# Optimization experiments

Measured on AMD Instinct MI355X. Metric: run time of the kernel, lower is better.

The kernel has to match this reference:

```python
import jax, jax.numpy as jnp
import numpy as np

D_MODEL = 128
N_HEADS = 8
D_HEAD = D_MODEL // N_HEADS
D_EDGE = 32
D_GATE = max(D_EDGE * 2, 64)
N_NODES = 50000
N_EDGES = 800000


def setup_inputs() -> dict:
    key = jax.random.key(0)
    ks = jax.random.split(key, 11)
    s = 1.0 / np.sqrt(D_MODEL)
    se = 1.0 / np.sqrt(D_EDGE)
    sg = 1.0 / np.sqrt(D_GATE)
    return {
        "x": jax.random.normal(ks[0], (N_NODES, D_MODEL), jnp.float32),
        "edge_index": jax.random.randint(ks[1], (2, N_EDGES), 0, N_NODES, jnp.int64) if jax.config.jax_enable_x64 else jax.random.randint(ks[1], (2, N_EDGES), 0, N_NODES, jnp.int32),
        "edge_attr": jax.random.normal(ks[2], (N_EDGES, D_EDGE), jnp.float32),
        "W_q": jax.random.normal(ks[3], (D_MODEL, D_MODEL), jnp.float32) * s,
        "W_k": jax.random.normal(ks[4], (D_MODEL, D_MODEL), jnp.float32) * s,
        "W_v": jax.random.normal(ks[5], (D_MODEL, D_MODEL), jnp.float32) * s,
        "W_o": jax.random.normal(ks[6], (D_MODEL, D_MODEL), jnp.float32) * s,
        "W_ek": jax.random.normal(ks[7], (D_EDGE, D_MODEL), jnp.float32) * se,
        "W_ev": jax.random.normal(ks[8], (D_EDGE, D_MODEL), jnp.float32) * se,
        "W_g1": jax.random.normal(ks[9], (D_EDGE, D_GATE), jnp.float32) * se,
        "W_g2": jax.random.normal(ks[10], (D_GATE, N_HEADS), jnp.float32) * sg,
    }


def reference(x, edge_index, edge_attr, W_q, W_k, W_v, W_o, W_ek, W_ev, W_g1, W_g2):
    N = x.shape[0]
    E = edge_attr.shape[0]
    H, D = N_HEADS, D_HEAD
    src, dst = edge_index[0], edge_index[1]

    q = (x @ W_q).reshape(N, H, D)
    k = (x @ W_k).reshape(N, H, D)
    v = (x @ W_v).reshape(N, H, D)

    # per-edge gather + edge-feature enrichment of K, V
    q_e = q[dst]                                        # [E,H,D]
    k_e = k[src] + (edge_attr @ W_ek).reshape(E, H, D)  # [E,H,D]
    v_e = v[src] + (edge_attr @ W_ev).reshape(E, H, D)  # [E,H,D]

    scale = jnp.asarray(np.sqrt(D), x.dtype)
    gate = jax.nn.silu(edge_attr @ W_g1) @ W_g2         # [E,H]
    scores = jnp.sum(q_e * k_e, axis=-1) / scale + gate  # [E,H]

    # 3-pass scatter segment softmax over destination nodes
    m = jax.ops.segment_max(scores, dst, num_segments=N)   # [N,H]
    exp_s = jnp.exp(scores - m[dst])                        # [E,H]
    denom = jax.ops.segment_sum(exp_s, dst, num_segments=N)  # [N,H]
    att = exp_s / (denom[dst] + 1e-9)                       # [E,H]

    out = jax.ops.segment_sum(att[..., None] * v_e, dst, num_segments=N)  # [N,H,D]
    return out.reshape(N, H * D) @ W_o
```

## Files before the change

kernel.cpp:

```cpp
#include <hip/hip_runtime.h>

#define NN 50000
#define NP 50048
#define NE 800000
#define DM 128
#define NH 8
#define DE 32
#define DG 64
#define MAXDEG 64
#define LOG2E 1.44269504088896f
#define SHIFT 16.0f

typedef __attribute__((ext_vector_type(8))) short bf16x8;
typedef __attribute__((ext_vector_type(4))) float f32x4;

__device__ __forceinline__ unsigned short f2bf(float f) {
    unsigned u = __float_as_uint(f);
    unsigned r = u + 0x7FFFu + ((u >> 16) & 1u);
    return (unsigned short)(r >> 16);
}

__device__ __forceinline__ float red16(float x) {
    float v = x;
    int t;
    t = __builtin_amdgcn_update_dpp(0, __float_as_int(v), 0xB1, 0xF, 0xF, true);
    v += __int_as_float(t);
    t = __builtin_amdgcn_update_dpp(0, __float_as_int(v), 0x4E, 0xF, 0xF, true);
    v += __int_as_float(t);
    t = __builtin_amdgcn_update_dpp(0, __float_as_int(v), 0x141, 0xF, 0xF, true);
    v += __int_as_float(t);
    t = __builtin_amdgcn_update_dpp(0, __float_as_int(v), 0x140, 0xF, 0xF, true);
    v += __int_as_float(t);
    return v;
}

__global__ void k_prep(const float* __restrict__ x, unsigned short* __restrict__ xh,
                       const float* __restrict__ Wq, const float* __restrict__ Wk,
                       const float* __restrict__ Wv, unsigned short* __restrict__ wt,
                       const float* __restrict__ Wo, unsigned short* __restrict__ wto,
                       const float* __restrict__ Wek, float* __restrict__ WekT,
                       int* __restrict__ cnt) {
    int idx = blockIdx.x * 256 + threadIdx.x;
    if (idx < NP * DM / 4) {
        float4 t = (idx < NN * DM / 4) ? ((const float4*)x)[idx] : make_float4(0.f, 0.f, 0.f, 0.f);
        ushort4 o;
        o.x = f2bf(t.x); o.y = f2bf(t.y); o.z = f2bf(t.z); o.w = f2bf(t.w);
        ((ushort4*)xh)[idx] = o;
    }
    if (idx < 3 * DM * DM) {
        int m = idx >> 14, rem = idx & 16383, c = rem >> 7, kk = rem & 127;
        const float* W = m == 0 ? Wq : (m == 1 ? Wk : Wv);
        wt[idx] = f2bf(W[kk * DM + c]);
    }
    if (idx < DM * DM) {
        int c = idx >> 7, kk = idx & 127;
        wto[idx] = f2bf(Wo[kk * DM + c]);
    }
    if (idx < DE * DM) {
        int d = idx >> 5, i = idx & 31;
        WekT[idx] = Wek[i * DM + d];
    }
    if (idx < NN) cnt[idx] = 0;
}

__global__ __launch_bounds__(256) void k_qkv(
    const unsigned short* __restrict__ xh, const unsigned short* __restrict__ wt,
    float* __restrict__ q, unsigned* __restrict__ kvp) {
    int lane = threadIdx.x & 63;
    int w = threadIdx.x >> 6;
    int rt = blockIdx.x * 64 + w * 16;
    int cl = lane & 15;
    int kc = (lane >> 4) * 8;
    bf16x8 a[4];
    #pragma unroll
    for (int ks = 0; ks < 4; ++ks)
        a[ks] = *(const bf16x8*)(xh + (size_t)(rt + cl) * DM + ks * 32 + kc);
    int r0w = rt + (lane >> 4) * 4;
    #pragma unroll
    for (int m = 0; m < 3; ++m) {
        const unsigned short* wtm = wt + m * DM * DM;
        f32x4 acc[8];
        #pragma unroll
        for (int j = 0; j < 8; ++j) acc[j] = (f32x4){0.f, 0.f, 0.f, 0.f};
        #pragma unroll
        for (int j = 0; j < 8; ++j) {
            #pragma unroll
            for (int ks = 0; ks < 4; ++ks) {
                bf16x8 b = *(const bf16x8*)(wtm + (size_t)(j * 16 + cl) * DM + ks * 32 + kc);
                acc[j] = __builtin_amdgcn_mfma_f32_16x16x32_bf16(a[ks], b, acc[j], 0, 0, 0);
            }
        }
        if (m == 0) {
            #pragma unroll
            for (int j = 0; j < 8; ++j)
                #pragma unroll
                for (int r = 0; r < 4; ++r)
                    q[(size_t)(r0w + r) * DM + j * 16 + cl] = acc[j][r];
        } else {
            #pragma unroll
            for (int j = 0; j < 4; ++j)
                #pragma unroll
                for (int r = 0; r < 4; ++r) {
                    unsigned pk = (unsigned)f2bf(acc[j][r]) | ((unsigned)f2bf(acc[j + 4][r]) << 16);
                    kvp[(size_t)(r0w + r) * DM + 2 * (j * 16 + cl) + (m - 1)] = pk;
                }
        }
    }
}

__global__ __launch_bounds__(256) void k_qwek(
    const float* __restrict__ q, const float* __restrict__ WekT,
    unsigned* __restrict__ qwekh) {
    int t = threadIdx.x & 127;
    int sub = threadIdx.x >> 7;
    int h = t >> 4, i2 = t & 15;
    float wk0[16], wk1[16];
    #pragma unroll
    for (int d = 0; d < 16; ++d) {
        wk0[d] = WekT[(h * 16 + d) * 32 + 2 * i2];
        wk1[d] = WekT[(h * 16 + d) * 32 + 2 * i2 + 1];
    }
    for (int n = blockIdx.x * 2 + sub; n < NN; n += gridDim.x * 2) {
        const float4* qr = (const float4*)(q + (size_t)n * DM + h * 16);
        float a0 = 0.f, a1 = 0.f;
        #pragma unroll
        for (int c = 0; c < 4; ++c) {
            float4 qq = qr[c];
            a0 += qq.x * wk0[4*c] + qq.y * wk0[4*c+1] + qq.z * wk0[4*c+2] + qq.w * wk0[4*c+3];
            a1 += qq.x * wk1[4*c] + qq.y * wk1[4*c+1] + qq.z * wk1[4*c+2] + qq.w * wk1[4*c+3];
        }
        a0 *= (0.25f * LOG2E);
        a1 *= (0.25f * LOG2E);
        qwekh[(size_t)n * 128 + h * 16 + i2] = (unsigned)f2bf(a0) | ((unsigned)f2bf(a1) << 16);
    }
}

__global__ __launch_bounds__(256) void k_edge(
    const float* __restrict__ ea,
    const float* __restrict__ Wg1, const float* __restrict__ Wg2,
    const int* __restrict__ ei, int* __restrict__ cnt,
    int2* __restrict__ eb, float2* __restrict__ g2) {
    int e = blockIdx.x * 256 + threadIdx.x;
    float eav[DE];
    {
        const float4* p4 = (const float4*)(ea + (size_t)e * DE);
        #pragma unroll
        for (int c = 0; c < DE / 4; ++c) {
            float4 t = p4[c];
            eav[4*c+0] = t.x; eav[4*c+1] = t.y; eav[4*c+2] = t.z; eav[4*c+3] = t.w;
        }
    }
    float out[NH] = {0.f, 0.f, 0.f, 0.f, 0.f, 0.f, 0.f, 0.f};
    #pragma unroll
    for (int half = 0; half < 2; ++half) {
        const int j0 = half * 32;
        float acc[32];
        #pragma unroll
        for (int j = 0; j < 32; ++j) acc[j] = 0.f;
        #pragma unroll 2
        for (int i = 0; i < DE; ++i) {
            const float* __restrict__ wrow = Wg1 + i * DG + j0;
            float a = eav[i];
            #pragma unroll
            for (int j = 0; j < 32; ++j) acc[j] += a * wrow[j];
        }
        #pragma unroll 2
        for (int j = 0; j < 32; ++j) {
            float h = acc[j];
            float s = __fdividef(h, 1.f + __expf(-h));
            const float* __restrict__ w2r = Wg2 + (j0 + j) * NH;
            #pragma unroll
            for (int hh = 0; hh < NH; ++hh) out[hh] += s * w2r[hh];
        }
    }
    #pragma unroll
    for (int hh = 0; hh < 4; ++hh)
        g2[(size_t)e * 4 + hh] = make_float2(out[hh] * LOG2E - SHIFT, out[hh + 4] * LOG2E - SHIFT);
    int src = ei[e], dst = ei[NE + e];
    int slot = atomicAdd(&cnt[dst], 1);
    if (slot < MAXDEG) eb[(size_t)dst * MAXDEG + slot] = make_int2(e, src);
}

#define ECOMP(KV, EAV, G, QA, QB, QWA, QWB, LA, LB, AA, AB, E0, E1, E2, E3) {     \
    unsigned kw = (unsigned)(KV), vw = (unsigned)((KV) >> 32);                    \
    float kA = __uint_as_float(kw << 16);                                         \
    float kB = __uint_as_float(kw & 0xFFFF0000u);                                 \
    float vA = __uint_as_float(vw << 16);                                         \
    float vB = __uint_as_float(vw & 0xFFFF0000u);                                 \
    float pA = QA * kA + EAV.x * QWA.x + EAV.y * QWA.y;                           \
    float pB = QB * kB + EAV.x * QWB.x + EAV.y * QWB.y;                           \
    pA = red16(pA);                                                               \
    pB = red16(pB);                                                               \
    float pxA = __builtin_amdgcn_exp2f(pA + G.x);                                 \
    float pxB = __builtin_amdgcn_exp2f(pB + G.y);                                 \
    LA += pxA;  LB += pxB;                                                        \
    AA += pxA * vA;  AB += pxB * vB;                                              \
    E0 += pxA * EAV.x;  E1 += pxA * EAV.y;                                        \
    E2 += pxB * EAV.x;  E3 += pxB * EAV.y;                                        \
}

#define LOADGEN(JIDX, EVV, SVV, KDST, EDST, GDST) {                               \
    int e_ = __builtin_amdgcn_readlane(EVV, JIDX);                                \
    int s_ = __builtin_amdgcn_readlane(SVV, JIDX);                                \
    KDST = kvp[(size_t)s_ * 64 + lane];                                           \
    EDST = *(const float2*)(ea + (size_t)e_ * DE + 2 * i2);                       \
    GDST = g2[(size_t)e_ * 4 + hA];                                               \
}

__global__ __launch_bounds__(256) void k_fused(
    const float* __restrict__ q, const unsigned long long* __restrict__ kvp,
    const unsigned* __restrict__ qwekh, const float2* __restrict__ g2,
    const float* __restrict__ ea, const int2* __restrict__ eb,
    const int* __restrict__ cnt, const float* __restrict__ Wev,
    float* __restrict__ outb) {
    int lane = threadIdx.x & 63;
    int gwid = blockIdx.x * 4 + (threadIdx.x >> 6);
    int n0 = gwid * 2, n1 = n0 + 1;
    int hA = lane >> 4;
    int i2 = lane & 15;
    const float QSC = 0.25f * LOG2E;

    int deg0 = cnt[n0]; deg0 = deg0 > MAXDEG ? MAXDEG : deg0;
    int deg1 = cnt[n1]; deg1 = deg1 > MAXDEG ? MAXDEG : deg1;
    int s0 = lane < deg0 ? lane : 0;
    int s1 = lane < deg1 ? lane : 0;
    int2 t0 = eb[(size_t)n0 * MAXDEG + s0];
    int2 t1 = eb[(size_t)n1 * MAXDEG + s1];
    if (deg0 == 0) { t0.x = 0; t0.y = 0; }
    if (deg1 == 0) { t1.x = 0; t1.y = 0; }
    int ev0 = t0.x, sv0 = t0.y, ev1 = t1.x, sv1 = t1.y;

    float qA0 = q[(size_t)n0 * DM + lane] * QSC, qB0 = q[(size_t)n0 * DM + 64 + lane] * QSC;
    float qA1 = q[(size_t)n1 * DM + lane] * QSC, qB1 = q[(size_t)n1 * DM + 64 + lane] * QSC;
    unsigned uA0 = qwekh[(size_t)n0 * 128 + hA * 16 + i2];
    unsigned uB0 = qwekh[(size_t)n0 * 128 + (hA + 4) * 16 + i2];
    unsigned uA1 = qwekh[(size_t)n1 * 128 + hA * 16 + i2];
    unsigned uB1 = qwekh[(size_t)n1 * 128 + (hA + 4) * 16 + i2];
    float2 qwA0 = make_float2(__uint_as_float(uA0 << 16), __uint_as_float(uA0 & 0xFFFF0000u));
    float2 qwB0 = make_float2(__uint_as_float(uB0 << 16), __uint_as_float(uB0 & 0xFFFF0000u));
    float2 qwA1 = make_float2(__uint_as_float(uA1 << 16), __uint_as_float(uA1 & 0xFFFF0000u));
    float2 qwB1 = make_float2(__uint_as_float(uB1 << 16), __uint_as_float(uB1 & 0xFFFF0000u));

    float lA0 = 0.f, lB0 = 0.f, aA0 = 0.f, aB0 = 0.f;
    float e00 = 0.f, e01 = 0.f, e02 = 0.f, e03 = 0.f;
    float lA1 = 0.f, lB1 = 0.f, aA1 = 0.f, aB1 = 0.f;
    float e10 = 0.f, e11 = 0.f, e12 = 0.f, e13 = 0.f;

    int degm = deg0 > deg1 ? deg0 : deg1;

    unsigned long long kvA0, kvA1, kvB0, kvB1;
    float2 eaA0, eaA1, eaB0, eaB1, gA0, gA1, gB0, gB1;
    LOADGEN(0, ev0, sv0, kvA0, eaA0, gA0)
    LOADGEN(0, ev1, sv1, kvA1, eaA1, gA1)
    LOADGEN(1, ev0, sv0, kvB0, eaB0, gB0)
    LOADGEN(1, ev1, sv1, kvB1, eaB1, gB1)

    for (int j = 0; j < degm; j += 2) {
        if (j < deg0) ECOMP(kvA0, eaA0, gA0, qA0, qB0, qwA0, qwB0, lA0, lB0, aA0, aB0, e00, e01, e02, e03)
        int jp = j + 2 < MAXDEG ? j + 2 : MAXDEG - 1;
        LOADGEN(jp, ev0, sv0, kvA0, eaA0, gA0)
        if (j < deg1) ECOMP(kvA1, eaA1, gA1, qA1, qB1, qwA1, qwB1, lA1, lB1, aA1, aB1, e10, e11, e12, e13)
        LOADGEN(jp, ev1, sv1, kvA1, eaA1, gA1)
        if (j + 1 < deg0) ECOMP(kvB0, eaB0, gB0, qA0, qB0, qwA0, qwB0, lA0, lB0, aA0, aB0, e00, e01, e02, e03)
        int jq = j + 3 < MAXDEG ? j + 3 : MAXDEG - 1;
        LOADGEN(jq, ev0, sv0, kvB0, eaB0, gB0)
        if (j + 1 < deg1) ECOMP(kvB1, eaB1, gB1, qA1, qB1, qwA1, qwB1, lA1, lB1, aA1, aB1, e10, e11, e12, e13)
        LOADGEN(jq, ev1, sv1, kvB1, eaB1, gB1)
    }

    int basel = lane & 48;
    float enA0 = 0.f, enB0 = 0.f, enA1 = 0.f, enB1 = 0.f;
    #pragma unroll
    for (int i = 0; i < DE; i += 2) {
        int sl = basel | (i >> 1);
        float w0A = Wev[i * DM + lane],      w1A = Wev[(i + 1) * DM + lane];
        float w0B = Wev[i * DM + 64 + lane], w1B = Wev[(i + 1) * DM + 64 + lane];
        enA0 += __shfl(e00, sl) * w0A + __shfl(e01, sl) * w1A;
        enB0 += __shfl(e02, sl) * w0B + __shfl(e03, sl) * w1B;
        enA1 += __shfl(e10, sl) * w0A + __shfl(e11, sl) * w1A;
        enB1 += __shfl(e12, sl) * w0B + __shfl(e13, sl) * w1B;
    }
    outb[(size_t)n0 * DM + lane]      = (aA0 + enA0) / fmaxf(lA0, 1e-30f);
    outb[(size_t)n0 * DM + 64 + lane] = (aB0 + enB0) / fmaxf(lB0, 1e-30f);
    outb[(size_t)n1 * DM + lane]      = (aA1 + enA1) / fmaxf(lA1, 1e-30f);
    outb[(size_t)n1 * DM + 64 + lane] = (aB1 + enB1) / fmaxf(lB1, 1e-30f);
}

__global__ __launch_bounds__(256) void k_final(
    float* __restrict__ dout, const unsigned short* __restrict__ wto) {
    int lane = threadIdx.x & 63;
    int w = threadIdx.x >> 6;
    int rt = blockIdx.x * 64 + w * 16;
    if (rt >= NN) return;
    int cl = lane & 15;
    int kc = (lane >> 4) * 8;
    bf16x8 a[4];
    #pragma unroll
    for (int ks = 0; ks < 4; ++ks) {
        float4 f0 = *(const float4*)(dout + (size_t)(rt + cl) * DM + ks * 32 + kc);
        float4 f1 = *(const float4*)(dout + (size_t)(rt + cl) * DM + ks * 32 + kc + 4);
        bf16x8 av;
        av[0] = (short)f2bf(f0.x); av[1] = (short)f2bf(f0.y);
        av[2] = (short)f2bf(f0.z); av[3] = (short)f2bf(f0.w);
        av[4] = (short)f2bf(f1.x); av[5] = (short)f2bf(f1.y);
        av[6] = (short)f2bf(f1.z); av[7] = (short)f2bf(f1.w);
        a[ks] = av;
    }
    f32x4 acc[8];
    #pragma unroll
    for (int j = 0; j < 8; ++j) acc[j] = (f32x4){0.f, 0.f, 0.f, 0.f};
    #pragma unroll
    for (int j = 0; j < 8; ++j) {
        #pragma unroll
        for (int ks = 0; ks < 4; ++ks) {
            bf16x8 b = *(const bf16x8*)(wto + (size_t)(j * 16 + cl) * DM + ks * 32 + kc);
            acc[j] = __builtin_amdgcn_mfma_f32_16x16x32_bf16(a[ks], b, acc[j], 0, 0, 0);
        }
    }
    int r0w = rt + (lane >> 4) * 4;
    #pragma unroll
    for (int j = 0; j < 8; ++j)
        #pragma unroll
        for (int r = 0; r < 4; ++r)
            dout[(size_t)(r0w + r) * DM + j * 16 + cl] = acc[j][r];
}

extern "C" void kernel_launch(void* const* d_in, const int* in_sizes, int n_in,
                              void* d_out, int out_size, void* d_ws, size_t ws_size,
                              hipStream_t stream) {
    const float* x   = (const float*)d_in[0];
    const int*   ei  = (const int*)d_in[1];
    const float* ea  = (const float*)d_in[2];
    const float* Wq  = (const float*)d_in[3];
    const float* Wk  = (const float*)d_in[4];
    const float* Wv  = (const float*)d_in[5];
    const float* Wo  = (const float*)d_in[6];
    const float* Wek = (const float*)d_in[7];
    const float* Wev = (const float*)d_in[8];
    const float* Wg1 = (const float*)d_in[9];
    const float* Wg2 = (const float*)d_in[10];
    float* dout = (float*)d_out;

    float* ws = (float*)d_ws;
    float* q        = ws;
    unsigned* kvp   = (unsigned*)(q + (size_t)NP * DM);
    unsigned* qwekh = kvp + (size_t)NP * DM;
    float2* g2      = (float2*)(qwekh + (size_t)NN * 128);
    int2* eb        = (int2*)(g2 + (size_t)NE * 4);
    int* cnt        = (int*)(eb + (size_t)NN * MAXDEG);
    unsigned short* xh = (unsigned short*)(cnt + NN);
    unsigned short* wt = xh + (size_t)NP * DM;
    unsigned short* wto = wt + 3 * DM * DM;
    float* WekT     = (float*)(wto + DM * DM);

    k_prep<<<(NP * DM / 4 + 255) / 256, 256, 0, stream>>>(x, xh, Wq, Wk, Wv, wt, Wo, wto, Wek, WekT, cnt);
    k_qkv<<<NP / 64, 256, 0, stream>>>(xh, wt, q, kvp);
    k_qwek<<<512, 256, 0, stream>>>(q, WekT, qwekh);
    k_edge<<<NE / 256, 256, 0, stream>>>(ea, Wg1, Wg2, ei, cnt, eb, g2);
    k_fused<<<NN / 8, 256, 0, stream>>>(q, (const unsigned long long*)kvp,
                                        qwekh, g2, ea, eb, cnt, Wev, dout);
    k_final<<<(NN + 63) / 64, 256, 0, stream>>>(dout, wto);
}
```

Before: 315.6 us.

## Compute edge gate MLP with MFMA and store bf16 edge_attr copy

The per-edge gate MLP (silu(ea@Wg1)@Wg2) moves from scalar per-thread FMAs to bf16 MFMA tiles, with an LDS swizzled staging of the hidden layer. The same kernel writes a bf16 copy of edge_attr that the fused attention kernel gathers instead of fp32, halving that gather traffic. The separate x->bf16 conversion pass is folded into k_qkv, and the q scaling is applied once at the QKV store instead of in later kernels. This trades gate and edge-feature precision (bf16) for fewer memory passes and less ALU work.

```diff
diff --git a/kernel.cpp b/kernel.cpp
--- a/kernel.cpp
+++ b/kernel.cpp
@@ -34,19 +34,14 @@
     return v;
 }
 
-__global__ void k_prep(const float* __restrict__ x, unsigned short* __restrict__ xh,
-                       const float* __restrict__ Wq, const float* __restrict__ Wk,
+__global__ void k_prep(const float* __restrict__ Wq, const float* __restrict__ Wk,
                        const float* __restrict__ Wv, unsigned short* __restrict__ wt,
                        const float* __restrict__ Wo, unsigned short* __restrict__ wto,
                        const float* __restrict__ Wek, float* __restrict__ WekT,
+                       const float* __restrict__ Wg1, unsigned short* __restrict__ wg1t,
+                       const float* __restrict__ Wg2, unsigned short* __restrict__ wg2t,
                        int* __restrict__ cnt) {
     int idx = blockIdx.x * 256 + threadIdx.x;
-    if (idx < NP * DM / 4) {
-        float4 t = (idx < NN * DM / 4) ? ((const float4*)x)[idx] : make_float4(0.f, 0.f, 0.f, 0.f);
-        ushort4 o;
-        o.x = f2bf(t.x); o.y = f2bf(t.y); o.z = f2bf(t.z); o.w = f2bf(t.w);
-        ((ushort4*)xh)[idx] = o;
-    }
     if (idx < 3 * DM * DM) {
         int m = idx >> 14, rem = idx & 16383, c = rem >> 7, kk = rem & 127;
         const float* W = m == 0 ? Wq : (m == 1 ? Wk : Wv);
@@ -60,22 +55,44 @@
         int d = idx >> 5, i = idx & 31;
         WekT[idx] = Wek[i * DM + d];
     }
+    if (idx < DG * DE) {
+        int c = idx >> 5, kk = idx & 31;
+        wg1t[idx] = f2bf(Wg1[kk * DG + c]);
+    }
+    if (idx < 16 * DG) {
+        int c = idx >> 6, kk = idx & 63;
+        wg2t[idx] = (c < NH) ? f2bf(Wg2[kk * NH + c]) : (unsigned short)0;
+    }
     if (idx < NN) cnt[idx] = 0;
 }
 
 __global__ __launch_bounds__(256) void k_qkv(
-    const unsigned short* __restrict__ xh, const unsigned short* __restrict__ wt,
+    const float* __restrict__ x, const unsigned short* __restrict__ wt,
     float* __restrict__ q, unsigned* __restrict__ kvp) {
     int lane = threadIdx.x & 63;
     int w = threadIdx.x >> 6;
     int rt = blockIdx.x * 64 + w * 16;
     int cl = lane & 15;
     int kc = (lane >> 4) * 8;
+    bool valid = (rt + cl) < NN;
     bf16x8 a[4];
     #pragma unroll
-    for (int ks = 0; ks < 4; ++ks)
-        a[ks] = *(const bf16x8*)(xh + (size_t)(rt + cl) * DM + ks * 32 + kc);
+    for (int ks = 0; ks < 4; ++ks) {
+        float4 f0 = make_float4(0.f, 0.f, 0.f, 0.f), f1 = f0;
+        if (valid) {
+            const float* xp = x + (size_t)(rt + cl) * DM + ks * 32 + kc;
+            f0 = *(const float4*)xp;
+            f1 = *(const float4*)(xp + 4);
+        }
+        bf16x8 av;
+        av[0] = (short)f2bf(f0.x); av[1] = (short)f2bf(f0.y);
+        av[2] = (short)f2bf(f0.z); av[3] = (short)f2bf(f0.w);
+        av[4] = (short)f2bf(f1.x); av[5] = (short)f2bf(f1.y);
+        av[6] = (short)f2bf(f1.z); av[7] = (short)f2bf(f1.w);
+        a[ks] = av;
+    }
     int r0w = rt + (lane >> 4) * 4;
+    const float QSC = 0.25f * LOG2E;
     #pragma unroll
     for (int m = 0; m < 3; ++m) {
         const unsigned short* wtm = wt + m * DM * DM;
@@ -95,7 +112,7 @@
             for (int j = 0; j < 8; ++j)
                 #pragma unroll
                 for (int r = 0; r < 4; ++r)
-                    q[(size_t)(r0w + r) * DM + j * 16 + cl] = acc[j][r];
+                    q[(size_t)(r0w + r) * DM + j * 16 + cl] = acc[j][r] * QSC;
         } else {
             #pragma unroll
             for (int j = 0; j < 4; ++j)
@@ -129,88 +146,111 @@
             a0 += qq.x * wk0[4*c] + qq.y * wk0[4*c+1] + qq.z * wk0[4*c+2] + qq.w * wk0[4*c+3];
             a1 += qq.x * wk1[4*c] + qq.y * wk1[4*c+1] + qq.z * wk1[4*c+2] + qq.w * wk1[4*c+3];
         }
-        a0 *= (0.25f * LOG2E);
-        a1 *= (0.25f * LOG2E);
         qwekh[(size_t)n * 128 + h * 16 + i2] = (unsigned)f2bf(a0) | ((unsigned)f2bf(a1) << 16);
     }
 }
 
 __global__ __launch_bounds__(256) void k_edge(
     const float* __restrict__ ea,
-    const float* __restrict__ Wg1, const float* __restrict__ Wg2,
+    const unsigned short* __restrict__ wg1t, const unsigned short* __restrict__ wg2t,
     const int* __restrict__ ei, int* __restrict__ cnt,
-    int2* __restrict__ eb, float2* __restrict__ g2) {
-    int e = blockIdx.x * 256 + threadIdx.x;
-    float eav[DE];
-    {
-        const float4* p4 = (const float4*)(ea + (size_t)e * DE);
-        #pragma unroll
-        for (int c = 0; c < DE / 4; ++c) {
-            float4 t = p4[c];
-            eav[4*c+0] = t.x; eav[4*c+1] = t.y; eav[4*c+2] = t.z; eav[4*c+3] = t.w;
-        }
-    }
-    float out[NH] = {0.f, 0.f, 0.f, 0.f, 0.f, 0.f, 0.f, 0.f};
-    #pragma unroll
-    for (int half = 0; half < 2; ++half) {
-        const int j0 = half * 32;
-        float acc[32];
-        #pragma unroll
-        for (int j = 0; j < 32; ++j) acc[j] = 0.f;
-        #pragma unroll 2
-        for (int i = 0; i < DE; ++i) {
-            const float* __restrict__ wrow = Wg1 + i * DG + j0;
-            float a = eav[i];
-            #pragma unroll
-            for (int j = 0; j < 32; ++j) acc[j] += a * wrow[j];
-        }
-        #pragma unroll 2
-        for (int j = 0; j < 32; ++j) {
-            float h = acc[j];
-            float s = __fdividef(h, 1.f + __expf(-h));
-            const float* __restrict__ w2r = Wg2 + (j0 + j) * NH;
-            #pragma unroll
-            for (int hh = 0; hh < NH; ++hh) out[hh] += s * w2r[hh];
-        }
-    }
-    #pragma unroll
-    for (int hh = 0; hh < 4; ++hh)
-        g2[(size_t)e * 4 + hh] = make_float2(out[hh] * LOG2E - SHIFT, out[hh + 4] * LOG2E - SHIFT);
-    int src = ei[e], dst = ei[NE + e];
-    int slot = atomicAdd(&cnt[dst], 1);
-    if (slot < MAXDEG) eb[(size_t)dst * MAXDEG + slot] = make_int2(e, src);
-}
-
-#define ECOMP(KV, EAV, G, QA, QB, QWA, QWB, LA, LB, AA, AB, E0, E1, E2, E3) {     \
+    int2* __restrict__ eb, float2* __restrict__ g2, unsigned* __restrict__ eah) {
+    __shared__ unsigned short hls[4][16 * 64];
+    int lane = threadIdx.x & 63;
+    int wv = threadIdx.x >> 6;
+    int e0 = (blockIdx.x * 4 + wv) * 16;
+    int cl = lane & 15;
+    int g = lane >> 4;
+    int kc = g * 8;
+
+    const float* ear = ea + (size_t)(e0 + cl) * DE + kc;
+    float4 f0 = *(const float4*)ear;
+    float4 f1 = *(const float4*)(ear + 4);
+    bf16x8 a;
+    a[0] = (short)f2bf(f0.x); a[1] = (short)f2bf(f0.y);
+    a[2] = (short)f2bf(f0.z); a[3] = (short)f2bf(f0.w);
+    a[4] = (short)f2bf(f1.x); a[5] = (short)f2bf(f1.y);
+    a[6] = (short)f2bf(f1.z); a[7] = (short)f2bf(f1.w);
+    *(bf16x8*)(eah + (size_t)(e0 + cl) * 16 + kc / 2) = a;
+
+    f32x4 hC[4];
+    #pragma unroll
+    for (int j = 0; j < 4; ++j) {
+        bf16x8 b = *(const bf16x8*)(wg1t + (size_t)(j * 16 + cl) * DE + kc);
+        hC[j] = __builtin_amdgcn_mfma_f32_16x16x32_bf16(a, b, (f32x4){0.f, 0.f, 0.f, 0.f}, 0, 0, 0);
+    }
+
+    unsigned short* hw = hls[wv];
+    #pragma unroll
+    for (int j = 0; j < 4; ++j) {
+        #pragma unroll
+        for (int r = 0; r < 4; ++r) {
+            float h = hC[j][r];
+            float s = h * __frcp_rn(1.f + __builtin_amdgcn_exp2f(-LOG2E * h));
+            int rowE = g * 4 + r;
+            int byte = ((rowE * 128) + (j * 16 + cl) * 2) ^ ((rowE & 7) << 4);
+            *(unsigned short*)((char*)hw + byte) = f2bf(s);
+        }
+    }
+    __syncthreads();
+
+    int rb0 = ((cl * 128) + g * 16) ^ ((cl & 7) << 4);
+    int rb1 = ((cl * 128) + 64 + g * 16) ^ ((cl & 7) << 4);
+    bf16x8 a2lo = *(bf16x8*)((char*)hw + rb0);
+    bf16x8 a2hi = *(bf16x8*)((char*)hw + rb1);
+    bf16x8 b2lo = *(const bf16x8*)(wg2t + (size_t)cl * DG + kc);
+    bf16x8 b2hi = *(const bf16x8*)(wg2t + (size_t)cl * DG + 32 + kc);
+    f32x4 c2 = __builtin_amdgcn_mfma_f32_16x16x32_bf16(a2lo, b2lo, (f32x4){0.f, 0.f, 0.f, 0.f}, 0, 0, 0);
+    c2 = __builtin_amdgcn_mfma_f32_16x16x32_bf16(a2hi, b2hi, c2, 0, 0, 0);
+
+    #pragma unroll
+    for (int r = 0; r < 4; ++r) {
+        float val = c2[r] * LOG2E - SHIFT;
+        float other = __shfl_xor(val, 4);
+        if (cl < 4)
+            g2[(size_t)(e0 + g * 4 + r) * 4 + cl] = make_float2(val, other);
+    }
+
+    if (lane < 16) {
+        int e = e0 + lane;
+        int src = ei[e], dst = ei[NE + e];
+        int slot = atomicAdd(&cnt[dst], 1);
+        if (slot < MAXDEG) eb[(size_t)dst * MAXDEG + slot] = make_int2(e, src);
+    }
+}
+
+#define ECOMP(KV, EAU, G, QA, QB, QWA, QWB, LA, LB, AA, AB, E0, E1, E2, E3) {     \
     unsigned kw = (unsigned)(KV), vw = (unsigned)((KV) >> 32);                    \
     float kA = __uint_as_float(kw << 16);                                         \
     float kB = __uint_as_float(kw & 0xFFFF0000u);                                 \
     float vA = __uint_as_float(vw << 16);                                         \
     float vB = __uint_as_float(vw & 0xFFFF0000u);                                 \
-    float pA = QA * kA + EAV.x * QWA.x + EAV.y * QWA.y;                           \
-    float pB = QB * kB + EAV.x * QWB.x + EAV.y * QWB.y;                           \
+    float eax = __uint_as_float((EAU) << 16);                                     \
+    float eay = __uint_as_float((EAU) & 0xFFFF0000u);                             \
+    float pA = QA * kA + eax * QWA.x + eay * QWA.y;                               \
+    float pB = QB * kB + eax * QWB.x + eay * QWB.y;                               \
     pA = red16(pA);                                                               \
     pB = red16(pB);                                                               \
     float pxA = __builtin_amdgcn_exp2f(pA + G.x);                                 \
     float pxB = __builtin_amdgcn_exp2f(pB + G.y);                                 \
     LA += pxA;  LB += pxB;                                                        \
     AA += pxA * vA;  AB += pxB * vB;                                              \
-    E0 += pxA * EAV.x;  E1 += pxA * EAV.y;                                        \
-    E2 += pxB * EAV.x;  E3 += pxB * EAV.y;                                        \
+    E0 += pxA * eax;  E1 += pxA * eay;                                            \
+    E2 += pxB * eax;  E3 += pxB * eay;                                            \
 }
 
 #define LOADGEN(JIDX, EVV, SVV, KDST, EDST, GDST) {                               \
     int e_ = __builtin_amdgcn_readlane(EVV, JIDX);                                \
     int s_ = __builtin_amdgcn_readlane(SVV, JIDX);                                \
     KDST = kvp[(size_t)s_ * 64 + lane];                                           \
-    EDST = *(const float2*)(ea + (size_t)e_ * DE + 2 * i2);                       \
+    EDST = eah[(size_t)e_ * 16 + i2];                                             \
     GDST = g2[(size_t)e_ * 4 + hA];                                               \
 }
 
 __global__ __launch_bounds__(256) void k_fused(
     const float* __restrict__ q, const unsigned long long* __restrict__ kvp,
     const unsigned* __restrict__ qwekh, const float2* __restrict__ g2,
-    const float* __restrict__ ea, const int2* __restrict__ eb,
+    const unsigned* __restrict__ eah, const int2* __restrict__ eb,
     const int* __restrict__ cnt, const float* __restrict__ Wev,
     float* __restrict__ outb) {
     int lane = threadIdx.x & 63;
@@ -218,7 +258,6 @@
     int n0 = gwid * 2, n1 = n0 + 1;
     int hA = lane >> 4;
     int i2 = lane & 15;
-    const float QSC = 0.25f * LOG2E;
 
     int deg0 = cnt[n0]; deg0 = deg0 > MAXDEG ? MAXDEG : deg0;
     int deg1 = cnt[n1]; deg1 = deg1 > MAXDEG ? MAXDEG : deg1;
@@ -230,8 +269,8 @@
     if (deg1 == 0) { t1.x = 0; t1.y = 0; }
     int ev0 = t0.x, sv0 = t0.y, ev1 = t1.x, sv1 = t1.y;
 
-    float qA0 = q[(size_t)n0 * DM + lane] * QSC, qB0 = q[(size_t)n0 * DM + 64 + lane] * QSC;
-    float qA1 = q[(size_t)n1 * DM + lane] * QSC, qB1 = q[(size_t)n1 * DM + 64 + lane] * QSC;
+    float qA0 = q[(size_t)n0 * DM + lane], qB0 = q[(size_t)n0 * DM + 64 + lane];
+    float qA1 = q[(size_t)n1 * DM + lane], qB1 = q[(size_t)n1 * DM + 64 + lane];
     unsigned uA0 = qwekh[(size_t)n0 * 128 + hA * 16 + i2];
     unsigned uB0 = qwekh[(size_t)n0 * 128 + (hA + 4) * 16 + i2];
     unsigned uA1 = qwekh[(size_t)n1 * 128 + hA * 16 + i2];
@@ -249,20 +288,22 @@
     int degm = deg0 > deg1 ? deg0 : deg1;
 
     unsigned long long kvA0, kvA1, kvB0, kvB1;
-    float2 eaA0, eaA1, eaB0, eaB1, gA0, gA1, gB0, gB1;
+    unsigned eaA0, eaA1, eaB0, eaB1;
+    float2 gA0, gA1, gB0, gB1;
     LOADGEN(0, ev0, sv0, kvA0, eaA0, gA0)
     LOADGEN(0, ev1, sv1, kvA1, eaA1, gA1)
     LOADGEN(1, ev0, sv0, kvB0, eaB0, gB0)
     LOADGEN(1, ev1, sv1, kvB1, eaB1, gB1)
 
+    int jmax = degm - 1;
     for (int j = 0; j < degm; j += 2) {
         if (j < deg0) ECOMP(kvA0, eaA0, gA0, qA0, qB0, qwA0, qwB0, lA0, lB0, aA0, aB0, e00, e01, e02, e03)
-        int jp = j + 2 < MAXDEG ? j + 2 : MAXDEG - 1;
+        int jp = j + 2 < jmax ? j + 2 : jmax;
         LOADGEN(jp, ev0, sv0, kvA0, eaA0, gA0)
         if (j < deg1) ECOMP(kvA1, eaA1, gA1, qA1, qB1, qwA1, qwB1, lA1, lB1, aA1, aB1, e10, e11, e12, e13)
         LOADGEN(jp, ev1, sv1, kvA1, eaA1, gA1)
         if (j + 1 < deg0) ECOMP(kvB0, eaB0, gB0, qA0, qB0, qwA0, qwB0, lA0, lB0, aA0, aB0, e00, e01, e02, e03)
-        int jq = j + 3 < MAXDEG ? j + 3 : MAXDEG - 1;
+        int jq = j + 3 < jmax ? j + 3 : jmax;
         LOADGEN(jq, ev0, sv0, kvB0, eaB0, gB0)
         if (j + 1 < deg1) ECOMP(kvB1, eaB1, gB1, qA1, qB1, qwA1, qwB1, lA1, lB1, aA1, aB1, e10, e11, e12, e13)
         LOADGEN(jq, ev1, sv1, kvB1, eaB1, gB1)
@@ -347,17 +388,20 @@
     unsigned* qwekh = kvp + (size_t)NP * DM;
     float2* g2      = (float2*)(qwekh + (size_t)NN * 128);
     int2* eb        = (int2*)(g2 + (size_t)NE * 4);
-    int* cnt        = (int*)(eb + (size_t)NN * MAXDEG);
-    unsigned short* xh = (unsigned short*)(cnt + NN);
-    unsigned short* wt = xh + (size_t)NP * DM;
+    unsigned* eah   = (unsigned*)(eb + (size_t)NN * MAXDEG);
+    int* cnt        = (int*)(eah + (size_t)NE * 16);
+    unsigned short* wt = (unsigned short*)(cnt + NN);
     unsigned short* wto = wt + 3 * DM * DM;
-    float* WekT     = (float*)(wto + DM * DM);
-
-    k_prep<<<(NP * DM / 4 + 255) / 256, 256, 0, stream>>>(x, xh, Wq, Wk, Wv, wt, Wo, wto, Wek, WekT, cnt);
-    k_qkv<<<NP / 64, 256, 0, stream>>>(xh, wt, q, kvp);
+    unsigned short* wg1t = wto + DM * DM;
+    unsigned short* wg2t = wg1t + DG * DE;
+    float* WekT     = (float*)(wg2t + 16 * DG);
+
+    k_prep<<<(NN + 255) / 256, 256, 0, stream>>>(Wq, Wk, Wv, wt, Wo, wto, Wek, WekT,
+                                                 Wg1, wg1t, Wg2, wg2t, cnt);
+    k_qkv<<<NP / 64, 256, 0, stream>>>(x, wt, q, kvp);
     k_qwek<<<512, 256, 0, stream>>>(q, WekT, qwekh);
-    k_edge<<<NE / 256, 256, 0, stream>>>(ea, Wg1, Wg2, ei, cnt, eb, g2);
+    k_edge<<<NE / 64, 256, 0, stream>>>(ea, wg1t, wg2t, ei, cnt, eb, g2, eah);
     k_fused<<<NN / 8, 256, 0, stream>>>(q, (const unsigned long long*)kvp,
-                                        qwekh, g2, ea, eb, cnt, Wev, dout);
+                                        qwekh, g2, eah, eb, cnt, Wev, dout);
     k_final<<<(NN + 63) / 64, 256, 0, stream>>>(dout, wto);
 }
```

Result: faster. 279.6 us (-11.4%).
